# Optimization experiments

Hardware: AMD Instinct MI355X
Metric: run time of the kernel (lower is better)

Reference implementation:

```python
import jax, jax.numpy as jnp
import numpy as np


def _ln(x, g, b, eps=1e-5):
    m = x.mean(-1, keepdims=True)
    v = x.var(-1, keepdims=True)
    return (x - m) / jnp.sqrt(v + eps) * g + b


def setup_inputs() -> dict:
    key = jax.random.key(0)
    ks = jax.random.split(key, 12)
    B, N, F, D, DI = 1024, 100000, 128, 256, 512

    def w(k, shape, fan_in):
        return jax.random.normal(k, shape, jnp.float32) / np.sqrt(fan_in).astype(np.float32)

    return {
        "x_num": jax.random.normal(ks[0], (B, F), jnp.float32),
        "cand_num": jax.random.normal(ks[1], (N, F), jnp.float32),
        "cand_y": jax.random.normal(ks[2], (N, 1), jnp.float32),
        "W_lin": w(ks[3], (F, D), F), "b_lin": jnp.zeros(D, jnp.float32),
        "W_K": w(ks[4], (D, D), D), "b_K": jnp.zeros(D, jnp.float32),
        "W_Y": w(ks[5], (1, D), 2), "b_Y": jnp.zeros(D, jnp.float32),
        "W_T1": w(ks[6], (D, DI), D), "b_T1": jnp.zeros(DI, jnp.float32),
        "W_T2": w(ks[7], (DI, D), DI),
        "ln_p_g": jnp.ones(D, jnp.float32), "ln_p_b": jnp.zeros(D, jnp.float32),
        "W_P1": w(ks[8], (D, DI), D), "b_P1": jnp.zeros(DI, jnp.float32),
        "W_P2": w(ks[9], (DI, D), DI), "b_P2": jnp.zeros(D, jnp.float32),
        "ln_o_g": jnp.ones(D, jnp.float32), "ln_o_b": jnp.zeros(D, jnp.float32),
        "W_out": w(ks[10], (D, 1), D), "b_out": jnp.zeros(1, jnp.float32),
        "context_size": 96,
    }


def reference(x_num, cand_num, cand_y,
              W_lin, b_lin, W_K, b_K, W_Y, b_Y,
              W_T1, b_T1, W_T2,
              ln_p_g, ln_p_b, W_P1, b_P1, W_P2, b_P2,
              ln_o_g, ln_o_b, W_out, b_out,
              context_size):
    # Encoder (encoder_n_blocks=0, normlization=None -> identity f)
    x_enc = x_num @ W_lin + b_lin                       # [B, D]
    k = x_enc @ W_K + b_K                               # [B, D]
    # Candidate keys (computed under torch.no_grad in the original)
    ki_all = jax.lax.stop_gradient((cand_num @ W_lin + b_lin) @ W_K + b_K)  # [N, D]

    # Exact brute-force L2 kNN == faiss.IndexFlatL2
    d2 = (k * k).sum(-1, keepdims=True) - 2.0 * (k @ ki_all.T) + (ki_all * ki_all).sum(-1)  # [B, N]
    _, I = jax.lax.top_k(-d2, context_size)             # [B, C] ascending distance
    ki = ki_all[I]                                      # [B, C, D]

    # S = ||k - ki||^2 per the source formula; softmax over context
    S = (k * k).sum(-1, keepdims=True) \
        - 2.0 * jnp.einsum('bd,bcd->bc', k, ki) \
        + (ki * ki).sum(-1)                             # [B, C]
    weights = jax.nn.softmax(S, axis=-1)                # context_dropout=0 (eval)

    encode_y = cand_y[I] @ W_Y + b_Y                    # [B, C, D]
    diff = k[:, None, :] - ki                           # [B, C, D]
    V = encode_y + jax.nn.relu(diff @ W_T1 + b_T1) @ W_T2  # T MLP, no bias on 2nd linear
    V = jnp.einsum('bc,bcd->bd', weights, V)            # weighted context reduction

    x = x_enc + V
    # predictor residual block: LN -> Linear -> ReLU -> Linear
    h = _ln(x, ln_p_g, ln_p_b)
    x = x + (jax.nn.relu(h @ W_P1 + b_P1) @ W_P2 + b_P2)
    # head P: LN -> ReLU -> Linear(d, 1)
    return jax.nn.relu(_ln(x, ln_o_g, ln_o_b)) @ W_out + b_out  # [B, 1]
```

## Files before the change

kernel.cpp:

```cpp
#include <hip/hip_runtime.h>
#include <math.h>

#define BQ 1024
#define FDIM 128
#define DDIM 256
#define DIDIM 512
#define NTOT 100000
#define NP 100096
#define CTX 96
#define CAP 8192
#define MSUB 12288
#define RSUB 48
#define LBUF 1536

typedef _Float16 f16x8 __attribute__((ext_vector_type(8)));
typedef _Float16 f16x4 __attribute__((ext_vector_type(4)));
typedef _Float16 f16x2 __attribute__((ext_vector_type(2)));
typedef float f32x4 __attribute__((ext_vector_type(4)));

__global__ __launch_bounds__(256) void k_fuse(
    const float* __restrict__ Wlin, const float* __restrict__ blin,
    const float* __restrict__ WK, const float* __restrict__ bK,
    float* __restrict__ Wf, float* __restrict__ bf)
{
    __shared__ float red[256];
    int i = blockIdx.x, j = threadIdx.x;
    if (i < FDIM) {
        float acc = 0.f;
        for (int l = 0; l < DDIM; ++l) acc += Wlin[i*DDIM + l] * WK[l*DDIM + j];
        Wf[i*DDIM + j] = acc;
    } else {
        float acc = bK[j];
        for (int l = 0; l < DDIM; ++l) acc += blin[l] * WK[l*DDIM + j];
        bf[j] = acc;
        red[j] = acc*acc; __syncthreads();
        for (int s2 = 128; s2 > 0; s2 >>= 1) { if (j < s2) red[j] += red[j+s2]; __syncthreads(); }
        if (j == 0) bf[256] = red[0];
    }
}

__global__ __launch_bounds__(256) void k_fuse2(
    const float* __restrict__ Wf, const float* __restrict__ WT1, float* __restrict__ WfT1)
{
    __shared__ float wr[DDIM];
    int i = blockIdx.x, j = threadIdx.x;
    wr[j] = Wf[i*DDIM + j];
    __syncthreads();
    float a0 = 0.f, a1 = 0.f;
    for (int l = 0; l < DDIM; ++l) {
        float w = wr[l];
        a0 += w * WT1[(size_t)l*DIDIM + j];
        a1 += w * WT1[(size_t)l*DIDIM + j + 256];
    }
    WfT1[(size_t)i*DIDIM + j] = a0;
    WfT1[(size_t)i*DIDIM + j + 256] = a1;
}

__global__ __launch_bounds__(128) void k_cvt_w(
    const float* __restrict__ Wf, const float* __restrict__ WfT1, _Float16* __restrict__ Wsp)
{
    int j = blockIdx.x, l = threadIdx.x;
    float w = (j < DDIM) ? Wf[l*DDIM + j] : WfT1[(size_t)l*DIDIM + (j - DDIM)];
    _Float16 h = (_Float16)w;
    float hf = (float)h;
    Wsp[(size_t)j*384 + l]       = h;
    Wsp[(size_t)j*384 + 128 + l] = (_Float16)((w - hf) * 64.f);
    Wsp[(size_t)j*384 + 256 + l] = (_Float16)(hf * 0.015625f);
}

__global__ __launch_bounds__(256) void k_query(
    const float* __restrict__ x, const float* __restrict__ Wlin,
    const float* __restrict__ blin, const float* __restrict__ Wf,
    const float* __restrict__ bf,
    float* __restrict__ xenc, float* __restrict__ kq)
{
    __shared__ float xs[FDIM];
    int b = blockIdx.x, j = threadIdx.x;
    if (j < FDIM) xs[j] = x[(size_t)b*FDIM + j];
    __syncthreads();
    float a0 = blin[j], a1 = bf[j];
    for (int l = 0; l < FDIM; ++l) {
        float xv = xs[l];
        a0 += xv * Wlin[l*DDIM + j];
        a1 += xv * Wf[l*DDIM + j];
    }
    xenc[(size_t)b*DDIM + j] = a0;
    kq[(size_t)b*DDIM + j] = a1;
}

__global__ __launch_bounds__(128) void k_kp(
    const float* __restrict__ kq, const float* __restrict__ Wf, float* __restrict__ kp)
{
    __shared__ float ks[DDIM];
    int b = blockIdx.x, l = threadIdx.x;
    ks[l] = kq[(size_t)b*DDIM + l];
    ks[l+128] = kq[(size_t)b*DDIM + l + 128];
    __syncthreads();
    float a = 0.f;
    for (int d = 0; d < DDIM; ++d) a += Wf[l*DDIM + d] * ks[d];
    kp[(size_t)b*FDIM + l] = a;
}

__global__ __launch_bounds__(256) void k_xp(
    const float* __restrict__ x, const float* __restrict__ WfT1,
    const float* __restrict__ bT1, float* __restrict__ xP)
{
    __shared__ float xs[FDIM];
    int b = blockIdx.x, j = threadIdx.x;
    if (j < FDIM) xs[j] = x[(size_t)b*FDIM + j];
    __syncthreads();
    float a0 = bT1[j], a1 = bT1[j + 256];
    for (int l = 0; l < FDIM; ++l) {
        float xv = xs[l];
        a0 += xv * WfT1[(size_t)l*DIDIM + j];
        a1 += xv * WfT1[(size_t)l*DIDIM + j + 256];
    }
    xP[(size_t)b*DIDIM + j] = a0;
    xP[(size_t)b*DIDIM + j + 256] = a1;
}

__global__ __launch_bounds__(256) void k_cvt_kp(
    const float* __restrict__ kp, _Float16* __restrict__ kp2)
{
    int t = blockIdx.x*256 + threadIdx.x;
    int row = t >> 5;
    int c4 = (t & 31) * 4;
    float4 v = *(const float4*)(kp + (size_t)row*FDIM + c4);
    float vv[4] = {v.x, v.y, v.z, v.w};
    f16x4 h, hs, l;
    #pragma unroll
    for (int q = 0; q < 4; ++q) {
        _Float16 hq = (_Float16)vv[q];
        float hf = (float)hq;
        h[q]  = hq;
        hs[q] = (_Float16)(hf * 0.015625f);
        l[q]  = (_Float16)((vv[q] - hf) * 64.f);
    }
    size_t b = (size_t)row*384 + c4;
    *(f16x4*)(kp2 + b)       = h;
    *(f16x4*)(kp2 + b + 128) = l;
    *(f16x4*)(kp2 + b + 256) = hs;
}

__global__ __launch_bounds__(256) void k_cvt_cand(
    const float* __restrict__ cand, _Float16* __restrict__ c2)
{
    int t = blockIdx.x*256 + threadIdx.x;
    int row = t >> 5;
    int c4 = (t & 31) * 4;
    float4 v = {0.f, 0.f, 0.f, 0.f};
    if (row < NTOT) v = *(const float4*)(cand + (size_t)row*FDIM + c4);
    float vv[4] = {v.x, v.y, v.z, v.w};
    f16x4 h, hs, l;
    #pragma unroll
    for (int q = 0; q < 4; ++q) {
        _Float16 hq = (_Float16)vv[q];
        float hf = (float)hq;
        h[q]  = hq;
        hs[q] = (_Float16)(hf * 0.015625f);
        l[q]  = (_Float16)((vv[q] - hf) * 64.f);
    }
    size_t b = (size_t)row*384 + c4;
    *(f16x4*)(c2 + b)       = h;
    *(f16x4*)(c2 + b + 128) = hs;
    *(f16x4*)(c2 + b + 256) = l;
}

template<int MODE>
__global__ __launch_bounds__(256) void k_csplit(
    const _Float16* __restrict__ A, const _Float16* __restrict__ B,
    _Float16* __restrict__ P, float* __restrict__ knp, const float* __restrict__ bf)
{
    __shared__ __align__(16) _Float16 As[128*64];
    __shared__ __align__(16) _Float16 Bs[128*64];
    int tid = threadIdx.x;
    int lane = tid & 63, wv = tid >> 6;
    int wm = wv >> 1, wn = wv & 1;
    int bm, bn;
    if (MODE == 0) {
        int r = blockIdx.x & 7, u2 = blockIdx.x >> 3;
        int pq = r*391 + u2;
        bn = (pq & 3) * 128;
        bm = (pq >> 2) * 128;
    } else {
        bn = blockIdx.x * 128;
        bm = blockIdx.y * 128;
    }
    f32x4 acc[4][4] = {};
    const size_t baseA = (size_t)bm * 384;
    const size_t baseB = (size_t)bn * 384;
    const int NKT = (MODE == 0) ? 2 : 6;
    for (int kt = 0; kt < NKT; ++kt) {
        #pragma unroll
        for (int r = 0; r < 4; ++r) {
            int w = wv*4 + r;
            int s = w*64 + lane;
            int rl = s & 15;
            int q  = (s >> 4) & 3;
            int kk2= (s >> 6) & 1;
            int ii = (s >> 7) & 3;
            int wq = (s >> 9) & 1;
            size_t goff = (size_t)(wq*64 + ii*16 + rl)*384 + kt*64 + (kk2*4 + q)*8;
            __builtin_amdgcn_global_load_lds(
                (const __attribute__((address_space(1))) void*)(A + baseA + goff),
                (__attribute__((address_space(3))) void*)(As + w*512), 16, 0, 0);
            __builtin_amdgcn_global_load_lds(
                (const __attribute__((address_space(1))) void*)(B + baseB + goff),
                (__attribute__((address_space(3))) void*)(Bs + w*512), 16, 0, 0);
        }
        __syncthreads();
        #pragma unroll
        for (int kk = 0; kk < 2; ++kk) {
            f16x8 af[4], bfr[4];
            #pragma unroll
            for (int i = 0; i < 4; ++i)
                af[i] = *(const f16x8*)&As[((wm*8 + i*2 + kk)*64 + (lane>>4)*16 + (lane&15))*8];
            #pragma unroll
            for (int j = 0; j < 4; ++j)
                bfr[j] = *(const f16x8*)&Bs[((wn*8 + j*2 + kk)*64 + (lane>>4)*16 + (lane&15))*8];
            #pragma unroll
            for (int i = 0; i < 4; ++i)
                #pragma unroll
                for (int j = 0; j < 4; ++j)
                    acc[i][j] = __builtin_amdgcn_mfma_f32_16x16x32_f16(af[i], bfr[j], acc[i][j], 0, 0, 0);
        }
        __syncthreads();
    }
    if (MODE == 0) {
        #pragma unroll
        for (int i = 0; i < 4; ++i) {
            int m = bm + wm*64 + i*16 + (lane>>4)*4;
            #pragma unroll
            for (int j = 0; j < 4; ++j) {
                int col = bn + wn*64 + j*16 + (lane&15);
                #pragma unroll
                for (int rg = 0; rg < 4; ++rg)
                    P[(size_t)(m + rg)*DIDIM + col] = (_Float16)acc[i][j][rg];
            }
        }
    } else {
        float bfv[4];
        #pragma unroll
        for (int j = 0; j < 4; ++j) bfv[j] = bf[bn + wn*64 + j*16 + (lane&15)];
        int bnt = bn >> 7;
        #pragma unroll
        for (int i = 0; i < 4; ++i) {
            #pragma unroll
            for (int rg = 0; rg < 4; ++rg) {
                float s = 0.f;
                #pragma unroll
                for (int j = 0; j < 4; ++j) {
                    float q = acc[i][j][rg];
                    s += q * (q + 2.f*bfv[j]);
                }
                s += __shfl_xor(s, 1, 64);
                s += __shfl_xor(s, 2, 64);
                s += __shfl_xor(s, 4, 64);
                s += __shfl_xor(s, 8, 64);
                if ((lane & 15) == 0) {
                    int row = bm + wm*64 + i*16 + (lane>>4)*4 + rg;
                    knp[(size_t)(bnt*2 + wn)*NP + row] = s;
                }
            }
        }
    }
}

__global__ __launch_bounds__(256) void k_norm_fin(
    const float* __restrict__ knp, const float* __restrict__ bf, float* __restrict__ kinorm)
{
    int n = blockIdx.x*256 + threadIdx.x;
    kinorm[n] = (n < NTOT)
        ? bf[256] + knp[n] + knp[(size_t)NP + n] + knp[(size_t)2*NP + n] + knp[(size_t)3*NP + n]
        : INFINITY;
}

__global__ __launch_bounds__(256) void k_mini(
    const _Float16* __restrict__ kp2, const _Float16* __restrict__ cand2,
    const float* __restrict__ kinorm, _Float16* __restrict__ msb)
{
    __shared__ __align__(16) _Float16 As[128*64];
    __shared__ __align__(16) _Float16 Bs[128*64];
    int tid = threadIdx.x;
    int lane = tid & 63, wv = tid >> 6;
    int wm = wv >> 1, wn = wv & 1;
    int bm = blockIdx.x * 128;
    int bn = blockIdx.y * 128;
    f32x4 acc[4][4] = {};
    const size_t baseA = (size_t)bm * 384;
    const size_t baseB = (size_t)bn * 384;
    for (int kt = 0; kt < 2; ++kt) {
        #pragma unroll
        for (int r = 0; r < 4; ++r) {
            int w = wv*4 + r;
            int s = w*64 + lane;
            int rl = s & 15;
            int q  = (s >> 4) & 3;
            int kk2= (s >> 6) & 1;
            int ii = (s >> 7) & 3;
            int wq = (s >> 9) & 1;
            size_t goff = (size_t)(wq*64 + ii*16 + rl)*384 + kt*64 + (kk2*4 + q)*8;
            __builtin_amdgcn_global_load_lds(
                (const __attribute__((address_space(1))) void*)(kp2 + baseA + goff),
                (__attribute__((address_space(3))) void*)(As + w*512), 16, 0, 0);
            __builtin_amdgcn_global_load_lds(
                (const __attribute__((address_space(1))) void*)(cand2 + baseB + goff),
                (__attribute__((address_space(3))) void*)(Bs + w*512), 16, 0, 0);
        }
        __syncthreads();
        #pragma unroll
        for (int kk = 0; kk < 2; ++kk) {
            f16x8 af[4], bfr[4];
            #pragma unroll
            for (int i = 0; i < 4; ++i)
                af[i] = *(const f16x8*)&As[((wm*8 + i*2 + kk)*64 + (lane>>4)*16 + (lane&15))*8];
            #pragma unroll
            for (int j = 0; j < 4; ++j)
                bfr[j] = *(const f16x8*)&Bs[((wn*8 + j*2 + kk)*64 + (lane>>4)*16 + (lane&15))*8];
            #pragma unroll
            for (int i = 0; i < 4; ++i)
                #pragma unroll
                for (int j = 0; j < 4; ++j)
                    acc[i][j] = __builtin_amdgcn_mfma_f32_16x16x32_f16(af[i], bfr[j], acc[i][j], 0, 0, 0);
        }
        __syncthreads();
    }
    #pragma unroll
    for (int i = 0; i < 4; ++i) {
        int m = bm + wm*64 + i*16 + (lane>>4)*4;
        #pragma unroll
        for (int j = 0; j < 4; ++j) {
            int nl = bn + wn*64 + j*16 + (lane&15);
            float kn = kinorm[nl];
            #pragma unroll
            for (int rg = 0; rg < 4; ++rg)
                msb[(size_t)(m + rg)*MSUB + nl] = (_Float16)fmaxf(kn - 2.f*acc[i][j][rg], 0.f);
        }
    }
}

__global__ __launch_bounds__(256) void k_subT(
    const unsigned short* __restrict__ msb, int* __restrict__ Tq)
{
    __shared__ unsigned h[1024];
    __shared__ unsigned pr[256];
    __shared__ unsigned h2[64];
    __shared__ int tstar;
    __shared__ unsigned cbel;
    int b = blockIdx.x, tid = threadIdx.x;
    #pragma unroll
    for (int i = 0; i < 4; ++i) h[tid + i*256] = 0;
    if (tid == 0) tstar = 1023;
    if (tid < 64) h2[tid] = 0;
    __syncthreads();
    const unsigned short* row = msb + (size_t)b*MSUB;
    for (int base = 0; base < MSUB; base += 2048) {
        uint4 u = *(const uint4*)(row + base + tid*8);
        atomicAdd(&h[(u.x & 0xffffu) >> 6], 1u);
        atomicAdd(&h[(u.x >> 16) >> 6], 1u);
        atomicAdd(&h[(u.y & 0xffffu) >> 6], 1u);
        atomicAdd(&h[(u.y >> 16) >> 6], 1u);
        atomicAdd(&h[(u.z & 0xffffu) >> 6], 1u);
        atomicAdd(&h[(u.z >> 16) >> 6], 1u);
        atomicAdd(&h[(u.w & 0xffffu) >> 6], 1u);
        atomicAdd(&h[(u.w >> 16) >> 6], 1u);
    }
    __syncthreads();
    unsigned s0 = h[tid*4], s1 = h[tid*4+1], s2 = h[tid*4+2], s3 = h[tid*4+3];
    unsigned tot = s0 + s1 + s2 + s3;
    pr[tid] = tot;
    __syncthreads();
    for (int off = 1; off < 256; off <<= 1) {
        unsigned t2 = (tid >= off) ? pr[tid - off] : 0;
        __syncthreads();
        pr[tid] += t2;
        __syncthreads();
    }
    unsigned c = pr[tid] - tot;
    int found = -1;
    c += s0; if (c >= RSUB) found = tid*4;
    if (found < 0) { c += s1; if (c >= RSUB) found = tid*4+1; }
    if (found < 0) { c += s2; if (c >= RSUB) found = tid*4+2; }
    if (found < 0) { c += s3; if (c >= RSUB) found = tid*4+3; }
    if (found >= 0) atomicMin(&tstar, found);
    __syncthreads();
    if (tid == (tstar >> 2)) {
        unsigned below = pr[tid] - tot;
        int pos = tstar & 3;
        if (pos > 0) below += s0;
        if (pos > 1) below += s1;
        if (pos > 2) below += s2;
        cbel = below;
    }
    __syncthreads();
    int ts = tstar;
    for (int base = 0; base < MSUB; base += 2048) {
        uint4 u = *(const uint4*)(row + base + tid*8);
        unsigned e[8] = { u.x & 0xffffu, u.x >> 16, u.y & 0xffffu, u.y >> 16,
                          u.z & 0xffffu, u.z >> 16, u.w & 0xffffu, u.w >> 16 };
        #pragma unroll
        for (int q = 0; q < 8; ++q)
            if ((int)(e[q] >> 6) == ts) atomicAdd(&h2[e[q] & 63], 1u);
    }
    __syncthreads();
    if (tid == 0) {
        unsigned cum = cbel; int code = 63;
        for (int i = 0; i < 64; ++i) { cum += h2[i]; if (cum >= RSUB) { code = i; break; } }
        Tq[b] = (ts << 6) + code;
    }
}

__global__ __launch_bounds__(256) void k_zero(int* __restrict__ cnt)
{
    int t = blockIdx.x*256 + threadIdx.x;
    if (t < BQ) cnt[t] = 0;
}

__global__ __launch_bounds__(256) void k_dist_mfma(
    const _Float16* __restrict__ kp2, const _Float16* __restrict__ cand2,
    const float* __restrict__ kinorm, const int* __restrict__ Tq,
    int* __restrict__ cnt, int* __restrict__ candI)
{
    __shared__ __align__(16) _Float16 As[128*64];
    __shared__ __align__(16) _Float16 Bs[128*64];
    __shared__ int lcnt;
    __shared__ unsigned lbuf[LBUF];
    int tid = threadIdx.x;
    int lane = tid & 63, wv = tid >> 6;
    int wm = wv >> 1, wn = wv & 1;
    int r0 = blockIdx.x & 7, u0 = blockIdx.x >> 3;
    int pq = r0*782 + u0;
    int bm = (pq & 7) * 128;
    int bn = (pq >> 3) * 128;
    if (tid == 0) lcnt = 0;
    f32x4 acc[4][4] = {};
    const size_t baseA = (size_t)bm * 384;
    const size_t baseB = (size_t)bn * 384;
    for (int kt = 0; kt < 2; ++kt) {
        #pragma unroll
        for (int r = 0; r < 4; ++r) {
            int w = wv*4 + r;
            int s = w*64 + lane;
            int rl = s & 15;
            int q  = (s >> 4) & 3;
            int kk2= (s >> 6) & 1;
            int ii = (s >> 7) & 3;
            int wq = (s >> 9) & 1;
            size_t goff = (size_t)(wq*64 + ii*16 + rl)*384 + kt*64 + (kk2*4 + q)*8;
            __builtin_amdgcn_global_load_lds(
                (const __attribute__((address_space(1))) void*)(kp2 + baseA + goff),
                (__attribute__((address_space(3))) void*)(As + w*512), 16, 0, 0);
            __builtin_amdgcn_global_load_lds(
                (const __attribute__((address_space(1))) void*)(cand2 + baseB + goff),
                (__attribute__((address_space(3))) void*)(Bs + w*512), 16, 0, 0);
        }
        __syncthreads();
        #pragma unroll
        for (int kk = 0; kk < 2; ++kk) {
            f16x8 af[4], bfr[4];
            #pragma unroll
            for (int i = 0; i < 4; ++i)
                af[i] = *(const f16x8*)&As[((wm*8 + i*2 + kk)*64 + (lane>>4)*16 + (lane&15))*8];
            #pragma unroll
            for (int j = 0; j < 4; ++j)
                bfr[j] = *(const f16x8*)&Bs[((wn*8 + j*2 + kk)*64 + (lane>>4)*16 + (lane&15))*8];
            #pragma unroll
            for (int i = 0; i < 4; ++i)
                #pragma unroll
                for (int j = 0; j < 4; ++j)
                    acc[i][j] = __builtin_amdgcn_mfma_f32_16x16x32_f16(af[i], bfr[j], acc[i][j], 0, 0, 0);
        }
        __syncthreads();
    }
    #pragma unroll
    for (int i = 0; i < 4; ++i) {
        int m0 = bm + wm*64 + i*16 + (lane>>4)*4;
        int tqs[4];
        #pragma unroll
        for (int rg = 0; rg < 4; ++rg) tqs[rg] = Tq[m0 + rg];
        #pragma unroll
        for (int j = 0; j < 4; ++j) {
            int nl = bn + wn*64 + j*16 + (lane&15);
            float kn = kinorm[nl];
            #pragma unroll
            for (int rg = 0; rg < 4; ++rg) {
                float sc = fmaxf(kn - 2.f*acc[i][j][rg], 0.f);
                _Float16 k16 = (_Float16)sc;
                unsigned short kb;
                __builtin_memcpy(&kb, &k16, 2);
                if (kb <= (unsigned short)tqs[rg]) {
                    int p = atomicAdd(&lcnt, 1);
                    if (p < LBUF) lbuf[p] = ((unsigned)(m0 + rg) << 17) | (unsigned)nl;
                    else {
                        int pp = atomicAdd(&cnt[m0 + rg], 1);
                        if (pp < CAP) candI[(size_t)(m0 + rg)*CAP + pp] = nl;
                    }
                }
            }
        }
    }
    __syncthreads();
    int c = lcnt < LBUF ? lcnt : LBUF;
    for (int i2 = tid; i2 < c; i2 += 256) {
        unsigned pk = lbuf[i2];
        int row = pk >> 17, col = (int)(pk & 0x1ffffu);
        int pp = atomicAdd(&cnt[row], 1);
        if (pp < CAP) candI[(size_t)row*CAP + pp] = col;
    }
}

__device__ __forceinline__ float row_score(
    const float* __restrict__ cand, const float* kps, const float* __restrict__ kinorm, int n)
{
    float acc0 = 0.f, acc1 = 0.f;
    #pragma unroll 4
    for (int d = 0; d < FDIM; d += 8) {
        float4 v0 = *(const float4*)(cand + (size_t)n*FDIM + d);
        float4 v1 = *(const float4*)(cand + (size_t)n*FDIM + d + 4);
        acc0 += v0.x*kps[d]   + v0.y*kps[d+1] + v0.z*kps[d+2] + v0.w*kps[d+3];
        acc1 += v1.x*kps[d+4] + v1.y*kps[d+5] + v1.z*kps[d+6] + v1.w*kps[d+7];
    }
    return kinorm[n] - 2.f*(acc0 + acc1);
}

__global__ __launch_bounds__(256) void k_fix(
    const float* __restrict__ kp, const float* __restrict__ cand,
    const float* __restrict__ kinorm, int* __restrict__ cnt, int* __restrict__ candI)
{
    __shared__ float kps[FDIM];
    __shared__ unsigned h[1024];
    __shared__ unsigned pr[256];
    __shared__ unsigned h2[64];
    __shared__ int tstar;
    __shared__ unsigned cbel;
    __shared__ unsigned Tsh;
    int b = blockIdx.x, tid = threadIdx.x;
    int c0 = cnt[b];
    if (c0 >= CTX && c0 <= CAP) return;
    if (tid < FDIM) kps[tid] = kp[(size_t)b*FDIM + tid];
    #pragma unroll
    for (int i = 0; i < 4; ++i) h[tid + i*256] = 0;
    if (tid == 0) tstar = 1023;
    if (tid < 64) h2[tid] = 0;
    __syncthreads();
    for (int n = tid; n < NTOT; n += 256) {
        float sc = fmaxf(row_score(cand, kps, kinorm, n), 0.f);
        _Float16 k16 = (_Float16)sc;
        unsigned short kb; __builtin_memcpy(&kb, &k16, 2);
        atomicAdd(&h[kb >> 6], 1u);
    }
    __syncthreads();
    unsigned s0 = h[tid*4], s1 = h[tid*4+1], s2 = h[tid*4+2], s3 = h[tid*4+3];
    unsigned tot = s0 + s1 + s2 + s3;
    pr[tid] = tot;
    __syncthreads();
    for (int off = 1; off < 256; off <<= 1) {
        unsigned t2 = (tid >= off) ? pr[tid - off] : 0;
        __syncthreads();
        pr[tid] += t2;
        __syncthreads();
    }
    unsigned c = pr[tid] - tot;
    int found = -1;
    c += s0; if (c >= CTX) found = tid*4;
    if (found < 0) { c += s1; if (c >= CTX) found = tid*4+1; }
    if (found < 0) { c += s2; if (c >= CTX) found = tid*4+2; }
    if (found < 0) { c += s3; if (c >= CTX) found = tid*4+3; }
    if (found >= 0) atomicMin(&tstar, found);
    __syncthreads();
    if (tid == (tstar >> 2)) {
        unsigned below = pr[tid] - tot;
        int pos = tstar & 3;
        if (pos > 0) below += s0;
        if (pos > 1) below += s1;
        if (pos > 2) below += s2;
        cbel = below;
    }
    __syncthreads();
    int ts = tstar;
    for (int n = tid; n < NTOT; n += 256) {
        float sc = fmaxf(row_score(cand, kps, kinorm, n), 0.f);
        _Float16 k16 = (_Float16)sc;
        unsigned short kb; __builtin_memcpy(&kb, &k16, 2);
        if ((int)((unsigned)kb >> 6) == ts) atomicAdd(&h2[kb & 63], 1u);
    }
    __syncthreads();
    if (tid == 0) {
        unsigned cum = cbel; int code = 63;
        for (int i = 0; i < 64; ++i) { cum += h2[i]; if (cum >= CTX) { code = i; break; } }
        Tsh = (unsigned)((ts << 6) + code);
        cnt[b] = 0;
    }
    __syncthreads();
    unsigned T2 = Tsh;
    for (int n = tid; n < NTOT; n += 256) {
        float sc = fmaxf(row_score(cand, kps, kinorm, n), 0.f);
        _Float16 k16 = (_Float16)sc;
        unsigned short kb; __builtin_memcpy(&kb, &k16, 2);
        if ((unsigned)kb <= T2) {
            int pp = atomicAdd(&cnt[b], 1);
            if (pp < CAP) candI[(size_t)b*CAP + pp] = n;
        }
    }
}

__global__ __launch_bounds__(256) void k_resc(
    const float* __restrict__ kp, const float* __restrict__ cand,
    const float* __restrict__ kinorm, const int* __restrict__ cnt,
    const int* __restrict__ candI,
    float* __restrict__ finV, int* __restrict__ finI)
{
    __shared__ float kps[FDIM];
    __shared__ float sval[2048];
    __shared__ int   sidx[2048];
    int b = blockIdx.x, tid = threadIdx.x;
    if (tid < FDIM) kps[tid] = kp[(size_t)b*FDIM + tid];
    if (tid < 128) { sval[tid] = INFINITY; sidx[tid] = 0x7fffffff; }
    int nc = cnt[b]; if (nc > CAP) nc = CAP;
    __syncthreads();
    for (int c0 = 0; c0 < nc; c0 += 1920) {
        int m = nc - c0; if (m > 1920) m = 1920;
        for (int c = tid; c < m; c += 256) {
            int n = candI[(size_t)b*CAP + c0 + c];
            sval[128 + c] = row_score(cand, kps, kinorm, n);
            sidx[128 + c] = n;
        }
        __syncthreads();
        int nv = 128 + m;
        int size = 256; while (size < nv) size <<= 1;
        for (int i2 = nv + tid; i2 < size; i2 += 256) { sval[i2] = INFINITY; sidx[i2] = 0x7fffffff; }
        __syncthreads();
        for (int k2 = 2; k2 <= size; k2 <<= 1) {
            for (int jj = k2 >> 1; jj > 0; jj >>= 1) {
                for (int i = tid; i < size; i += 256) {
                    int ix = i ^ jj;
                    if (ix > i) {
                        bool up = ((i & k2) == 0);
                        float a = sval[i], b2 = sval[ix];
                        int ia = sidx[i], ib = sidx[ix];
                        bool gt = (a > b2) || (a == b2 && ia > ib);
                        if (gt == up) {
                            sval[i] = b2; sval[ix] = a;
                            sidx[i] = ib; sidx[ix] = ia;
                        }
                    }
                }
                __syncthreads();
            }
        }
    }
    if (tid < CTX) { finV[(size_t)b*CTX + tid] = sval[tid]; finI[(size_t)b*CTX + tid] = sidx[tid]; }
}

__global__ __launch_bounds__(128) void k_weights(
    const float* __restrict__ finV, const int* __restrict__ finI,
    const float* __restrict__ candy, float* __restrict__ wts, float* __restrict__ wy)
{
    __shared__ float sh[128];
    int b = blockIdx.x, t = threadIdx.x;
    float v = (t < CTX) ? finV[b*CTX + t] : -INFINITY;
    sh[t] = v; __syncthreads();
    for (int s2 = 64; s2 > 0; s2 >>= 1) { if (t < s2) sh[t] = fmaxf(sh[t], sh[t+s2]); __syncthreads(); }
    float m = sh[0]; __syncthreads();
    float e = (t < CTX) ? expf(v - m) : 0.f;
    sh[t] = e; __syncthreads();
    for (int s2 = 64; s2 > 0; s2 >>= 1) { if (t < s2) sh[t] += sh[t+s2]; __syncthreads(); }
    float w = e / sh[0]; __syncthreads();
    if (t < CTX) wts[b*CTX + t] = w;
    float yv = (t < CTX) ? candy[finI[b*CTX + t]] : 0.f;
    sh[t] = w * yv; __syncthreads();
    for (int s2 = 64; s2 > 0; s2 >>= 1) { if (t < s2) sh[t] += sh[t+s2]; __syncthreads(); }
    if (t == 0) wy[b] = sh[0];
}

__global__ __launch_bounds__(256) void k_vgather(
    const float* __restrict__ xP, const _Float16* __restrict__ P,
    const int* __restrict__ finI, const float* __restrict__ wts,
    float* __restrict__ Hw)
{
    __shared__ float wsh[CTX];
    __shared__ int   idx[CTX];
    int b = blockIdx.x, tid = threadIdx.x;
    if (tid < CTX) { idx[tid] = finI[b*CTX + tid]; wsh[tid] = wts[b*CTX + tid]; }
    __syncthreads();
    int c0 = tid*2;
    float x0 = xP[(size_t)b*DIDIM + c0];
    float x1 = xP[(size_t)b*DIDIM + c0 + 1];
    float a0 = 0.f, a1 = 0.f;
    for (int c = 0; c < CTX; ++c) {
        size_t base = (size_t)idx[c]*DIDIM + c0;
        float w = wsh[c];
        f16x2 pv = *(const f16x2*)(P + base);
        a0 += w * fmaxf(x0 - (float)pv[0], 0.f);
        a1 += w * fmaxf(x1 - (float)pv[1], 0.f);
    }
    float2 r; r.x = a0; r.y = a1;
    *(float2*)(Hw + (size_t)b*DIDIM + c0) = r;
}

__device__ __forceinline__ float bsum(float v, float* red, int j)
{
    red[j] = v; __syncthreads();
    if (j < 64) {
        float t = red[j] + red[j+64] + red[j+128] + red[j+192];
        #pragma unroll
        for (int o2 = 32; o2; o2 >>= 1) t += __shfl_xor(t, o2, 64);
        if (j == 0) red[0] = t;
    }
    __syncthreads();
    float t = red[0];
    __syncthreads();
    return t;
}

__global__ __launch_bounds__(256) void k_final4(
    const float* __restrict__ xenc, const float* __restrict__ Hw,
    const float* __restrict__ wy,
    const float* __restrict__ WY, const float* __restrict__ bY,
    const float* __restrict__ WT2,
    const float* __restrict__ lpg, const float* __restrict__ lpb,
    const float* __restrict__ WP1, const float* __restrict__ bP1,
    const float* __restrict__ WP2, const float* __restrict__ bP2,
    const float* __restrict__ logg, const float* __restrict__ lob,
    const float* __restrict__ Wout, const float* __restrict__ bout,
    float* __restrict__ out)
{
    __shared__ float hs[4][DIDIM];
    __shared__ float xs[4][DDIM];
    __shared__ float red[256];
    int b0 = blockIdx.x*4, j = threadIdx.x;
    #pragma unroll
    for (int r = 0; r < 4; ++r) {
        hs[r][j] = Hw[(size_t)(b0+r)*DIDIM + j];
        hs[r][j+256] = Hw[(size_t)(b0+r)*DIDIM + j + 256];
    }
    __syncthreads();
    float v[4];
    #pragma unroll
    for (int r = 0; r < 4; ++r) v[r] = wy[b0+r]*WY[j] + bY[j];
    for (int dd = 0; dd < DIDIM; ++dd) {
        float w = WT2[dd*DDIM + j];
        #pragma unroll
        for (int r = 0; r < 4; ++r) v[r] += hs[r][dd]*w;
    }
    float x[4];
    #pragma unroll
    for (int r = 0; r < 4; ++r) x[r] = xenc[(size_t)(b0+r)*DDIM + j] + v[r];
    #pragma unroll
    for (int r = 0; r < 4; ++r) {
        float mean = bsum(x[r], red, j) * (1.f/DDIM);
        float xc = x[r] - mean;
        float var = bsum(xc*xc, red, j) * (1.f/DDIM);
        float rstd = 1.f / sqrtf(var + 1e-5f);
        xs[r][j] = xc * rstd * lpg[j] + lpb[j];
    }
    __syncthreads();
    float u0[4], u1[4];
    #pragma unroll
    for (int r = 0; r < 4; ++r) { u0[r] = bP1[j]; u1[r] = bP1[j+256]; }
    for (int dd = 0; dd < DDIM; ++dd) {
        float w0 = WP1[(size_t)dd*DIDIM + j], w1 = WP1[(size_t)dd*DIDIM + j + 256];
        #pragma unroll
        for (int r = 0; r < 4; ++r) { float hd = xs[r][dd]; u0[r] += hd*w0; u1[r] += hd*w1; }
    }
    __syncthreads();
    #pragma unroll
    for (int r = 0; r < 4; ++r) { hs[r][j] = fmaxf(u0[r], 0.f); hs[r][j+256] = fmaxf(u1[r], 0.f); }
    __syncthreads();
    float x2[4];
    #pragma unroll
    for (int r = 0; r < 4; ++r) x2[r] = x[r] + bP2[j];
    for (int dd = 0; dd < DIDIM; ++dd) {
        float w = WP2[dd*DDIM + j];
        #pragma unroll
        for (int r = 0; r < 4; ++r) x2[r] += hs[r][dd]*w;
    }
    #pragma unroll
    for (int r = 0; r < 4; ++r) {
        float mean = bsum(x2[r], red, j) * (1.f/DDIM);
        float xc = x2[r] - mean;
        float var = bsum(xc*xc, red, j) * (1.f/DDIM);
        float rstd = 1.f / sqrtf(var + 1e-5f);
        float rr = fmaxf(xc * rstd * logg[j] + lob[j], 0.f);
        float s = bsum(rr * Wout[j], red, j);
        if (j == 0) out[b0+r] = s + bout[0];
    }
}

extern "C" void kernel_launch(void* const* d_in, const int* in_sizes, int n_in,
                              void* d_out, int out_size, void* d_ws, size_t ws_size,
                              hipStream_t stream)
{
    (void)in_sizes; (void)n_in; (void)out_size; (void)ws_size;
    const float* x_num = (const float*)d_in[0];
    const float* cand  = (const float*)d_in[1];
    const float* candy = (const float*)d_in[2];
    const float* Wlin  = (const float*)d_in[3];
    const float* blin  = (const float*)d_in[4];
    const float* WK    = (const float*)d_in[5];
    const float* bK    = (const float*)d_in[6];
    const float* WY    = (const float*)d_in[7];
    const float* bY    = (const float*)d_in[8];
    const float* WT1   = (const float*)d_in[9];
    const float* bT1   = (const float*)d_in[10];
    const float* WT2   = (const float*)d_in[11];
    const float* lpg   = (const float*)d_in[12];
    const float* lpb   = (const float*)d_in[13];
    const float* WP1   = (const float*)d_in[14];
    const float* bP1   = (const float*)d_in[15];
    const float* WP2   = (const float*)d_in[16];
    const float* bP2   = (const float*)d_in[17];
    const float* logg  = (const float*)d_in[18];
    const float* lob   = (const float*)d_in[19];
    const float* Wout  = (const float*)d_in[20];
    const float* bout  = (const float*)d_in[21];
    float* out = (float*)d_out;

    float* ws = (float*)d_ws;
    size_t o = 0;
    float* Wf     = ws + o; o += (size_t)FDIM*DDIM;
    float* bf     = ws + o; o += 320;
    float* WfT1   = ws + o; o += (size_t)FDIM*DIDIM;
    float* xenc   = ws + o; o += (size_t)BQ*DDIM;
    float* kq     = ws + o; o += (size_t)BQ*DDIM;
    float* kp     = ws + o; o += (size_t)BQ*FDIM;
    float* kinorm = ws + o; o += NP;
    float* knp    = ws + o; o += (size_t)4*NP;
    float* finV   = ws + o; o += (size_t)BQ*CTX;
    int*   finI   = (int*)(ws + o); o += (size_t)BQ*CTX;
    float* wts    = ws + o; o += (size_t)BQ*CTX;
    float* wy     = ws + o; o += BQ;
    int*   Tq     = (int*)(ws + o); o += BQ;
    float* Hw     = ws + o; o += (size_t)BQ*DIDIM;
    float* xP     = ws + o; o += (size_t)BQ*DIDIM;
    _Float16* kp2 = (_Float16*)(ws + o); o += (size_t)BQ*384/2;
    _Float16* c2  = (_Float16*)(ws + o); o += (size_t)NP*384/2;
    _Float16* Wsp = (_Float16*)(ws + o); o += (size_t)768*384/2;
    int*   cnt    = (int*)(ws + o); o += BQ;
    int*   candI  = (int*)(ws + o); o += (size_t)BQ*CAP;
    _Float16* Pb  = (_Float16*)(ws + o); o += (size_t)NP*DIDIM/2;
    _Float16* P   = Pb;
    _Float16* msb = Pb;

    k_fuse<<<dim3(FDIM+1), dim3(256), 0, stream>>>(Wlin, blin, WK, bK, Wf, bf);
    k_fuse2<<<dim3(FDIM), dim3(256), 0, stream>>>(Wf, WT1, WfT1);
    k_cvt_w<<<dim3(DDIM+DIDIM), dim3(128), 0, stream>>>(Wf, WfT1, Wsp);
    k_query<<<dim3(BQ), dim3(256), 0, stream>>>(x_num, Wlin, blin, Wf, bf, xenc, kq);
    k_kp<<<dim3(BQ), dim3(128), 0, stream>>>(kq, Wf, kp);
    k_xp<<<dim3(BQ), dim3(256), 0, stream>>>(x_num, WfT1, bT1, xP);
    k_cvt_kp<<<dim3(BQ*FDIM/4/256), dim3(256), 0, stream>>>(kp, kp2);
    k_cvt_cand<<<dim3(NP*FDIM/4/256), dim3(256), 0, stream>>>(cand, c2);

    k_csplit<1><<<dim3(DDIM/128, NP/128), dim3(256), 0, stream>>>(c2, Wsp, (_Float16*)nullptr, knp, bf);
    k_norm_fin<<<dim3(NP/256), dim3(256), 0, stream>>>(knp, bf, kinorm);

    k_mini<<<dim3(BQ/128, MSUB/128), dim3(256), 0, stream>>>(kp2, c2, kinorm, msb);
    k_subT<<<dim3(BQ), dim3(256), 0, stream>>>((const unsigned short*)msb, Tq);

    k_zero<<<dim3(4), dim3(256), 0, stream>>>(cnt);
    k_dist_mfma<<<dim3((BQ/128)*(NP/128)), dim3(256), 0, stream>>>(kp2, c2, kinorm, Tq, cnt, candI);
    k_fix<<<dim3(BQ), dim3(256), 0, stream>>>(kp, cand, kinorm, cnt, candI);
    k_resc<<<dim3(BQ), dim3(256), 0, stream>>>(kp, cand, kinorm, cnt, candI, finV, finI);

    k_weights<<<dim3(BQ), dim3(128), 0, stream>>>(finV, finI, candy, wts, wy);

    k_csplit<0><<<dim3((NP/128)*(DIDIM/128)), dim3(256), 0, stream>>>(
        c2, Wsp + (size_t)DDIM*384, P, (float*)nullptr, (const float*)nullptr);
    k_vgather<<<dim3(BQ), dim3(256), 0, stream>>>(xP, P, finI, wts, Hw);
    k_final4<<<dim3(BQ/4), dim3(256), 0, stream>>>(xenc, Hw, wy, WY, bY, WT2,
                                                   lpg, lpb, WP1, bP1, WP2, bP2,
                                                   logg, lob, Wout, bout, out);
}
```

Baseline: 465.4 us.

## Load query fragments directly to registers and fold counter reset into threshold kernel

The distance kernel no longer stages the query tile in LDS. Each wave loads its A fragments straight from global memory into registers, and both K-slices of the candidate tile are issued up front into a double LDS buffer, so one barrier replaces the per-slice sync pairs. The separate zeroing kernel is dropped, and the per-query counter reset now happens inside the threshold kernel, which saves one launch. The cost is higher register pressure from holding 16 f16x8 A fragments, plus uncoalesced global reads for A, which is shared across wn waves and so gets re-read.

```diff
diff --git a/kernel.cpp b/kernel.cpp
--- a/kernel.cpp
+++ b/kernel.cpp
@@ -340,7 +340,7 @@
 }
 
 __global__ __launch_bounds__(256) void k_subT(
-    const unsigned short* __restrict__ msb, int* __restrict__ Tq)
+    const unsigned short* __restrict__ msb, int* __restrict__ Tq, int* __restrict__ cnt)
 {
     __shared__ unsigned h[1024];
     __shared__ unsigned pr[256];
@@ -348,6 +348,7 @@
     __shared__ int tstar;
     __shared__ unsigned cbel;
     int b = blockIdx.x, tid = threadIdx.x;
+    if (tid == 0) cnt[b] = 0;
     #pragma unroll
     for (int i = 0; i < 4; ++i) h[tid + i*256] = 0;
     if (tid == 0) tstar = 1023;
@@ -410,19 +411,12 @@
     }
 }
 
-__global__ __launch_bounds__(256) void k_zero(int* __restrict__ cnt)
-{
-    int t = blockIdx.x*256 + threadIdx.x;
-    if (t < BQ) cnt[t] = 0;
-}
-
 __global__ __launch_bounds__(256) void k_dist_mfma(
     const _Float16* __restrict__ kp2, const _Float16* __restrict__ cand2,
     const float* __restrict__ kinorm, const int* __restrict__ Tq,
     int* __restrict__ cnt, int* __restrict__ candI)
 {
-    __shared__ __align__(16) _Float16 As[128*64];
-    __shared__ __align__(16) _Float16 Bs[128*64];
+    __shared__ __align__(16) _Float16 Bs[2][128*64];
     __shared__ int lcnt;
     __shared__ unsigned lbuf[LBUF];
     int tid = threadIdx.x;
@@ -433,44 +427,45 @@
     int bm = (pq & 7) * 128;
     int bn = (pq >> 3) * 128;
     if (tid == 0) lcnt = 0;
-    f32x4 acc[4][4] = {};
-    const size_t baseA = (size_t)bm * 384;
     const size_t baseB = (size_t)bn * 384;
+    #pragma unroll
     for (int kt = 0; kt < 2; ++kt) {
         #pragma unroll
         for (int r = 0; r < 4; ++r) {
             int w = wv*4 + r;
             int s = w*64 + lane;
-            int rl = s & 15;
-            int q  = (s >> 4) & 3;
-            int kk2= (s >> 6) & 1;
-            int ii = (s >> 7) & 3;
-            int wq = (s >> 9) & 1;
+            int rl = s & 15, q = (s>>4)&3, kk2 = (s>>6)&1, ii = (s>>7)&3, wq = (s>>9)&1;
             size_t goff = (size_t)(wq*64 + ii*16 + rl)*384 + kt*64 + (kk2*4 + q)*8;
             __builtin_amdgcn_global_load_lds(
-                (const __attribute__((address_space(1))) void*)(kp2 + baseA + goff),
-                (__attribute__((address_space(3))) void*)(As + w*512), 16, 0, 0);
-            __builtin_amdgcn_global_load_lds(
                 (const __attribute__((address_space(1))) void*)(cand2 + baseB + goff),
-                (__attribute__((address_space(3))) void*)(Bs + w*512), 16, 0, 0);
-        }
-        __syncthreads();
+                (__attribute__((address_space(3))) void*)(Bs[kt] + w*512), 16, 0, 0);
+        }
+    }
+    f16x8 af[2][2][4];
+    #pragma unroll
+    for (int kt = 0; kt < 2; ++kt)
+        #pragma unroll
+        for (int kk = 0; kk < 2; ++kk)
+            #pragma unroll
+            for (int i = 0; i < 4; ++i)
+                af[kt][kk][i] = *(const f16x8*)&kp2[
+                    (size_t)(bm + wm*64 + i*16 + (lane&15))*384 + kt*64 + kk*32 + (lane>>4)*8];
+    f32x4 acc[4][4] = {};
+    __syncthreads();
+    #pragma unroll
+    for (int kt = 0; kt < 2; ++kt) {
         #pragma unroll
         for (int kk = 0; kk < 2; ++kk) {
-            f16x8 af[4], bfr[4];
-            #pragma unroll
-            for (int i = 0; i < 4; ++i)
-                af[i] = *(const f16x8*)&As[((wm*8 + i*2 + kk)*64 + (lane>>4)*16 + (lane&15))*8];
+            f16x8 bfr[4];
             #pragma unroll
             for (int j = 0; j < 4; ++j)
-                bfr[j] = *(const f16x8*)&Bs[((wn*8 + j*2 + kk)*64 + (lane>>4)*16 + (lane&15))*8];
+                bfr[j] = *(const f16x8*)&Bs[kt][((wn*8 + j*2 + kk)*64 + (lane>>4)*16 + (lane&15))*8];
             #pragma unroll
             for (int i = 0; i < 4; ++i)
                 #pragma unroll
                 for (int j = 0; j < 4; ++j)
-                    acc[i][j] = __builtin_amdgcn_mfma_f32_16x16x32_f16(af[i], bfr[j], acc[i][j], 0, 0, 0);
-        }
-        __syncthreads();
+                    acc[i][j] = __builtin_amdgcn_mfma_f32_16x16x32_f16(af[kt][kk][i], bfr[j], acc[i][j], 0, 0, 0);
+        }
     }
     #pragma unroll
     for (int i = 0; i < 4; ++i) {
@@ -855,9 +850,8 @@
     k_norm_fin<<<dim3(NP/256), dim3(256), 0, stream>>>(knp, bf, kinorm);
 
     k_mini<<<dim3(BQ/128, MSUB/128), dim3(256), 0, stream>>>(kp2, c2, kinorm, msb);
-    k_subT<<<dim3(BQ), dim3(256), 0, stream>>>((const unsigned short*)msb, Tq);
-
-    k_zero<<<dim3(4), dim3(256), 0, stream>>>(cnt);
+    k_subT<<<dim3(BQ), dim3(256), 0, stream>>>((const unsigned short*)msb, Tq, cnt);
+
     k_dist_mfma<<<dim3((BQ/128)*(NP/128)), dim3(256), 0, stream>>>(kp2, c2, kinorm, Tq, cnt, candI);
     k_fix<<<dim3(BQ), dim3(256), 0, stream>>>(kp, cand, kinorm, cnt, candI);
     k_resc<<<dim3(BQ), dim3(256), 0, stream>>>(kp, cand, kinorm, cnt, candI, finV, finI);
```

Result: slower. 475.1 us (+2.1%).
